# Kernel tuning notes

Hardware: AMD Instinct MI355X
Metric: run time of the kernel (lower is better)

Reference implementation:

```python
import jax, jax.numpy as jnp
import numpy as np

B, C, H, W = 8, 64, 64, 64
CK = C // 8  # query/key channels

def setup_inputs() -> dict:
    key = jax.random.key(0)
    ks = jax.random.split(key, 8)
    x = jax.random.normal(ks[0], (B, C, H, W), dtype=jnp.float32)
    # Conv1d with kernel size 1 == per-position linear map; store weights as [out, in].
    # (Spectral norm only rescales the weight matrix; with given weights the forward
    #  math is an ordinary 1x1 conv.)
    Wq = jax.random.normal(ks[1], (CK, C), dtype=jnp.float32) / np.sqrt(C)
    bq = jnp.zeros((CK,), dtype=jnp.float32)
    Wk = jax.random.normal(ks[2], (CK, C), dtype=jnp.float32) / np.sqrt(C)
    bk = jnp.zeros((CK,), dtype=jnp.float32)
    Wv = jax.random.normal(ks[3], (C, C), dtype=jnp.float32) / np.sqrt(C)
    bv = jnp.zeros((C,), dtype=jnp.float32)
    gamma = jnp.asarray(0.5, dtype=jnp.float32)  # nonzero so attention path matters
    return {"x": x, "Wq": Wq, "bq": bq, "Wk": Wk, "bk": bk, "Wv": Wv, "bv": bv, "gamma": gamma}

def reference(x, Wq, bq, Wk, bk, Wv, bv, gamma):
    b, c, h, w = x.shape
    flat = x.reshape(b, c, h * w)                       # [B, C, L]
    q = jnp.einsum('oc,bcl->blo', Wq, flat) + bq        # [B, L, C/8] (query permuted)
    k = jnp.einsum('oc,bcl->bol', Wk, flat) + bk[None, :, None]   # [B, C/8, L]
    v = jnp.einsum('oc,bcl->bol', Wv, flat) + bv[None, :, None]   # [B, C, L]
    qk = jnp.einsum('blo,bom->blm', q, k)               # [B, L, L]
    attn = jax.nn.softmax(qk, axis=1)                   # softmax over dim 1 (rows)
    out = jnp.einsum('bcl,blm->bcm', v, attn)           # [B, C, L]
    out = out.reshape(b, c, h, w)
    return gamma * out + x
```

## Files before the change

kernel.cpp:

```cpp
#include <hip/hip_runtime.h>
#include <math.h>

#define B_   8
#define C_   64
#define CK_  8
#define L_   4096

typedef __attribute__((ext_vector_type(8))) __bf16 bf16x8;
typedef __attribute__((ext_vector_type(4))) __bf16 bf16x4;
typedef __attribute__((ext_vector_type(4))) float  f32x4;

__global__ __launch_bounds__(256) void qkv_kernel(
    const float* __restrict__ x,
    const float* __restrict__ Wq, const float* __restrict__ bq,
    const float* __restrict__ Wk, const float* __restrict__ bk,
    const float* __restrict__ Wv, const float* __restrict__ bv,
    __bf16* __restrict__ qo, __bf16* __restrict__ ko, __bf16* __restrict__ vpack)
{
    __shared__ float LWq[CK_ * C_];
    __shared__ float LWk[CK_ * C_];
    __shared__ float LWv[C_ * C_];
    __shared__ __bf16 Lqs[64 * 8];
    __shared__ __bf16 Lks[64 * 8];

    const int tid = threadIdx.x;
    if (tid < 128) {
        ((float4*)LWq)[tid] = ((const float4*)Wq)[tid];
        ((float4*)LWk)[tid] = ((const float4*)Wk)[tid];
    }
    #pragma unroll
    for (int j = 0; j < 4; ++j)
        ((float4*)LWv)[tid + j * 256] = ((const float4*)Wv)[tid + j * 256];
    __syncthreads();

    const int b  = blockIdx.x >> 6;
    const int t  = blockIdx.x & 63;
    const int l0 = t << 6;
    const int lg = tid & 15;
    const int g  = tid >> 4;

    float va[4][4];
    float qk[4];
    #pragma unroll
    for (int j = 0; j < 4; ++j) {
        float bb = bv[4 * g + j];
        va[j][0] = bb; va[j][1] = bb; va[j][2] = bb; va[j][3] = bb;
    }
    {
        float bb = (g < 8) ? bq[g] : bk[g - 8];
        qk[0] = bb; qk[1] = bb; qk[2] = bb; qk[3] = bb;
    }
    const float* wqk = (g < 8) ? (LWq + g * C_) : (LWk + (g - 8) * C_);

    const float* xp = x + ((size_t)b * C_) * L_ + l0 + lg * 4;
    #pragma unroll 4
    for (int c4 = 0; c4 < 16; ++c4) {
        float4 xv[4];
        #pragma unroll
        for (int u = 0; u < 4; ++u)
            xv[u] = *(const float4*)(xp + (size_t)(4 * c4 + u) * L_);
        #pragma unroll
        for (int j = 0; j < 4; ++j) {
            float4 wv = ((const float4*)(LWv + (4 * g + j) * C_))[c4];
            float* a = va[j];
            a[0]=fmaf(wv.x,xv[0].x,a[0]); a[1]=fmaf(wv.x,xv[0].y,a[1]); a[2]=fmaf(wv.x,xv[0].z,a[2]); a[3]=fmaf(wv.x,xv[0].w,a[3]);
            a[0]=fmaf(wv.y,xv[1].x,a[0]); a[1]=fmaf(wv.y,xv[1].y,a[1]); a[2]=fmaf(wv.y,xv[1].z,a[2]); a[3]=fmaf(wv.y,xv[1].w,a[3]);
            a[0]=fmaf(wv.z,xv[2].x,a[0]); a[1]=fmaf(wv.z,xv[2].y,a[1]); a[2]=fmaf(wv.z,xv[2].z,a[2]); a[3]=fmaf(wv.z,xv[2].w,a[3]);
            a[0]=fmaf(wv.w,xv[3].x,a[0]); a[1]=fmaf(wv.w,xv[3].y,a[1]); a[2]=fmaf(wv.w,xv[3].z,a[2]); a[3]=fmaf(wv.w,xv[3].w,a[3]);
        }
        {
            float4 wv = ((const float4*)wqk)[c4];
            qk[0]=fmaf(wv.x,xv[0].x,qk[0]); qk[1]=fmaf(wv.x,xv[0].y,qk[1]); qk[2]=fmaf(wv.x,xv[0].z,qk[2]); qk[3]=fmaf(wv.x,xv[0].w,qk[3]);
            qk[0]=fmaf(wv.y,xv[1].x,qk[0]); qk[1]=fmaf(wv.y,xv[1].y,qk[1]); qk[2]=fmaf(wv.y,xv[1].z,qk[2]); qk[3]=fmaf(wv.y,xv[1].w,qk[3]);
            qk[0]=fmaf(wv.z,xv[2].x,qk[0]); qk[1]=fmaf(wv.z,xv[2].y,qk[1]); qk[2]=fmaf(wv.z,xv[2].z,qk[2]); qk[3]=fmaf(wv.z,xv[2].w,qk[3]);
            qk[0]=fmaf(wv.w,xv[3].x,qk[0]); qk[1]=fmaf(wv.w,xv[3].y,qk[1]); qk[2]=fmaf(wv.w,xv[3].z,qk[2]); qk[3]=fmaf(wv.w,xv[3].w,qk[3]);
        }
    }

    {
        __bf16* vt = vpack + ((size_t)b * 64 + t) * 4096;
        const int cb = g >> 2;
        const int sg = lg >> 2;
        const int qd = lg & 3;
        #pragma unroll
        for (int j = 0; j < 4; ++j) {
            bf16x4 vv;
            vv[0]=(__bf16)va[j][0]; vv[1]=(__bf16)va[j][1]; vv[2]=(__bf16)va[j][2]; vv[3]=(__bf16)va[j][3];
            *(bf16x4*)(vt + ((size_t)((cb * 4 + sg) * 64 + qd * 16 + (g & 3) * 4 + j)) * 4) = vv;
        }
    }
    #pragma unroll
    for (int u = 0; u < 4; ++u) {
        if (g < 8) Lqs[(lg * 4 + u) * 8 + g]       = (__bf16)qk[u];
        else       Lks[(lg * 4 + u) * 8 + (g - 8)] = (__bf16)qk[u];
    }
    __syncthreads();
    if (tid < 64) {
        *(bf16x8*)(qo + ((size_t)b * L_ + l0 + tid) * 8) = *(bf16x8*)(Lqs + tid * 8);
        *(bf16x8*)(ko + ((size_t)b * L_ + l0 + tid) * 8) = *(bf16x8*)(Lks + tid * 8);
    }
}

__global__ __launch_bounds__(512, 4) void attn_kernel(
    const __bf16* __restrict__ q, const __bf16* __restrict__ kT,
    const __bf16* __restrict__ VP, const float* __restrict__ x,
    const float* __restrict__ gamma_p, float* __restrict__ out)
{
    __shared__ __bf16 Lv[2][4][4096];
    __shared__ float  csA[8][16];

    const int tid  = threadIdx.x;
    const int w    = tid >> 6;
    const int lane = tid & 63;
    const int quad = lane >> 4;
    const int l16  = lane & 15;
    const int wh   = w & 3;
    const int lh   = w >> 2;
    const int mb   = blockIdx.x & 63;
    const int b    = blockIdx.x >> 6;
    const int m0   = mb << 6;

    const __bf16* vp = VP + (size_t)b * (64 * 4096);
    const __bf16* qb = q  + (size_t)b * L_ * CK_;

    bf16x8 kf = {};
    if (quad == 0) kf = *(const bf16x8*)(kT + ((size_t)b * L_ + m0 + wh * 16 + l16) * CK_);

    const __bf16* gk[4];
    int ok[4];
    #pragma unroll
    for (int k = 0; k < 4; ++k) {
        const int u = w * 4 + k, tl = u >> 3, seg = u & 7;
        gk[k] = vp + (size_t)((tl & 1) * 32 + (tl >> 1)) * 4096 + seg * 512 + lane * 8;
        ok[k] = tl * 4096 + seg * 512 + lane * 8;
    }

    f32x4 acc[4] = {};
    float csum = 0.f;
    bf16x8 r[4];

    #pragma unroll
    for (int k = 0; k < 4; ++k) r[k] = *(const bf16x8*)gk[k];
    #pragma unroll
    for (int k = 0; k < 4; ++k) *(bf16x8*)(&Lv[0][0][0] + ok[k]) = r[k];

    for (int i = 0; i < 16; ++i) {
        __syncthreads();

        if (i < 15) {
            #pragma unroll
            for (int k = 0; k < 4; ++k)
                r[k] = *(const bf16x8*)(gk[k] + (size_t)(i + 1) * 8192);
        }

        bf16x8 qA[4], qB[4];
        #pragma unroll
        for (int sg = 0; sg < 4; ++sg) {
            qA[sg] = *(const bf16x8*)(qb + (size_t)((lh * 32 + 2 * i)     * 64 + sg * 16 + l16) * CK_);
            qB[sg] = *(const bf16x8*)(qb + (size_t)((lh * 32 + 2 * i + 1) * 64 + sg * 16 + l16) * CK_);
        }

        bf16x4 pkA[4], pkB[4];
        #pragma unroll
        for (int sg = 0; sg < 4; ++sg) {
            f32x4 sv = __builtin_amdgcn_mfma_f32_16x16x32_bf16(qA[sg], kf, (f32x4){0.f,0.f,0.f,0.f}, 0, 0, 0);
            const float e0 = __expf(sv[0]);
            const float e1 = __expf(sv[1]);
            const float e2 = __expf(sv[2]);
            const float e3 = __expf(sv[3]);
            csum += (e0 + e1) + (e2 + e3);
            pkA[sg][0]=(__bf16)e0; pkA[sg][1]=(__bf16)e1; pkA[sg][2]=(__bf16)e2; pkA[sg][3]=(__bf16)e3;
        }
        #pragma unroll
        for (int sg = 0; sg < 4; ++sg) {
            f32x4 sv = __builtin_amdgcn_mfma_f32_16x16x32_bf16(qB[sg], kf, (f32x4){0.f,0.f,0.f,0.f}, 0, 0, 0);
            const float e0 = __expf(sv[0]);
            const float e1 = __expf(sv[1]);
            const float e2 = __expf(sv[2]);
            const float e3 = __expf(sv[3]);
            csum += (e0 + e1) + (e2 + e3);
            pkB[sg][0]=(__bf16)e0; pkB[sg][1]=(__bf16)e1; pkB[sg][2]=(__bf16)e2; pkB[sg][3]=(__bf16)e3;
        }

        const __bf16* LbA = &Lv[i & 1][lh][0];
        const __bf16* LbB = &Lv[i & 1][2 + lh][0];
        #pragma unroll
        for (int sg = 0; sg < 4; ++sg) {
            bf16x8 p8 = __builtin_shufflevector(pkA[sg], pkB[sg], 0, 1, 2, 3, 4, 5, 6, 7);
            #pragma unroll
            for (int cb = 0; cb < 4; ++cb) {
                bf16x4 vfA = *(const bf16x4*)(LbA + ((size_t)((cb * 4 + sg) * 64 + lane)) * 4);
                bf16x4 vfB = *(const bf16x4*)(LbB + ((size_t)((cb * 4 + sg) * 64 + lane)) * 4);
                bf16x8 a8 = __builtin_shufflevector(vfA, vfB, 0, 1, 2, 3, 4, 5, 6, 7);
                acc[cb] = __builtin_amdgcn_mfma_f32_16x16x32_bf16(a8, p8, acc[cb], 0, 0, 0);
            }
        }

        if (i < 15) {
            const int nb = (i + 1) & 1;
            #pragma unroll
            for (int k = 0; k < 4; ++k)
                *(bf16x8*)(&Lv[nb][0][0] + ok[k]) = r[k];
        }
    }

    float* Sc = (float*)&Lv[0][0][0];
    if (lh == 1) {
        #pragma unroll
        for (int cb = 0; cb < 4; ++cb)
            #pragma unroll
            for (int r2 = 0; r2 < 4; ++r2)
                Sc[(wh * 64 + cb * 16 + quad * 4 + r2) * 16 + l16] = acc[cb][r2];
    }
    csum += __shfl_xor(csum, 16);
    csum += __shfl_xor(csum, 32);
    if (quad == 0) csA[w][l16] = csum;
    __syncthreads();

    if (lh == 0) {
        const float rinv = gamma_p[0] / (csA[wh][l16] + csA[wh + 4][l16]);
        #pragma unroll
        for (int cb = 0; cb < 4; ++cb) {
            #pragma unroll
            for (int r2 = 0; r2 < 4; ++r2) {
                const int c = cb * 16 + quad * 4 + r2;
                const float vsum = acc[cb][r2] + Sc[(wh * 64 + c) * 16 + l16];
                const size_t idx = ((size_t)(b * 64 + c)) * L_ + m0 + wh * 16 + l16;
                out[idx] = fmaf(rinv, vsum, x[idx]);
            }
        }
    }
}

extern "C" void kernel_launch(void* const* d_in, const int* in_sizes, int n_in,
                              void* d_out, int out_size, void* d_ws, size_t ws_size,
                              hipStream_t stream) {
    const float* x  = (const float*)d_in[0];
    const float* Wq = (const float*)d_in[1];
    const float* bq = (const float*)d_in[2];
    const float* Wk = (const float*)d_in[3];
    const float* bk = (const float*)d_in[4];
    const float* Wv = (const float*)d_in[5];
    const float* bv = (const float*)d_in[6];
    const float* gm = (const float*)d_in[7];
    float* out = (float*)d_out;

    __bf16* ws    = (__bf16*)d_ws;
    __bf16* qo    = ws;
    __bf16* ko    = ws + 262144;
    __bf16* vpack = ws + 524288;

    qkv_kernel<<<dim3(B_ * (L_ / 64)), dim3(256), 0, stream>>>(
        x, Wq, bq, Wk, bk, Wv, bv, qo, ko, vpack);
    attn_kernel<<<dim3(B_ * 64), dim3(512), 0, stream>>>(
        qo, ko, vpack, x, gm, out);
}
```

Measured before the change: 126.8 us.

## Split attention l-range four ways with two m-tiles per wave

Reworks the attention kernel's wave decomposition. Each wave now computes two 16-column m-tiles, which lets one V fragment from LDS feed two MFMAs. The l dimension is split across four wave groups instead of two, each with its own private single-buffered LDS V slab, and partial results are reduced through shared memory at the end. This halves LDS V reads per MFMA but replaces double buffering with two barriers per iteration, adds a wider cross-group reduction, and raises register use.

```diff
diff --git a/kernel.cpp b/kernel.cpp
--- a/kernel.cpp
+++ b/kernel.cpp
@@ -106,16 +106,16 @@
     const __bf16* __restrict__ VP, const float* __restrict__ x,
     const float* __restrict__ gamma_p, float* __restrict__ out)
 {
-    __shared__ __bf16 Lv[2][4][4096];
-    __shared__ float  csA[8][16];
+    __shared__ __bf16 Lv[4][2][4096];
+    __shared__ float  csA[16][16];
 
     const int tid  = threadIdx.x;
     const int w    = tid >> 6;
     const int lane = tid & 63;
     const int quad = lane >> 4;
     const int l16  = lane & 15;
-    const int wh   = w & 3;
-    const int lh   = w >> 2;
+    const int wh   = w & 1;
+    const int lh   = w >> 1;
     const int mb   = blockIdx.x & 63;
     const int b    = blockIdx.x >> 6;
     const int m0   = mb << 6;
@@ -123,110 +123,123 @@
     const __bf16* vp = VP + (size_t)b * (64 * 4096);
     const __bf16* qb = q  + (size_t)b * L_ * CK_;
 
-    bf16x8 kf = {};
-    if (quad == 0) kf = *(const bf16x8*)(kT + ((size_t)b * L_ + m0 + wh * 16 + l16) * CK_);
-
-    const __bf16* gk[4];
-    int ok[4];
-    #pragma unroll
-    for (int k = 0; k < 4; ++k) {
-        const int u = w * 4 + k, tl = u >> 3, seg = u & 7;
-        gk[k] = vp + (size_t)((tl & 1) * 32 + (tl >> 1)) * 4096 + seg * 512 + lane * 8;
-        ok[k] = tl * 4096 + seg * 512 + lane * 8;
-    }
-
-    f32x4 acc[4] = {};
-    float csum = 0.f;
-    bf16x8 r[4];
-
-    #pragma unroll
-    for (int k = 0; k < 4; ++k) r[k] = *(const bf16x8*)gk[k];
-    #pragma unroll
-    for (int k = 0; k < 4; ++k) *(bf16x8*)(&Lv[0][0][0] + ok[k]) = r[k];
-
-    for (int i = 0; i < 16; ++i) {
-        __syncthreads();
-
-        if (i < 15) {
-            #pragma unroll
-            for (int k = 0; k < 4; ++k)
-                r[k] = *(const bf16x8*)(gk[k] + (size_t)(i + 1) * 8192);
-        }
-
+    bf16x8 kf0 = {}, kf1 = {};
+    if (quad == 0) {
+        kf0 = *(const bf16x8*)(kT + ((size_t)b * L_ + m0 + wh * 32 + l16) * CK_);
+        kf1 = *(const bf16x8*)(kT + ((size_t)b * L_ + m0 + wh * 32 + 16 + l16) * CK_);
+    }
+
+    const __bf16* gs = vp + ((size_t)(lh * 16 + wh)) * 4096 + lane * 8;
+    __bf16* Ld = &Lv[lh][wh][0] + lane * 8;
+
+    f32x4 acc0[4] = {}, acc1[4] = {};
+    float csum0 = 0.f, csum1 = 0.f;
+    bf16x8 r[8];
+
+    #pragma unroll
+    for (int k = 0; k < 8; ++k) r[k] = *(const bf16x8*)(gs + k * 512);
+    #pragma unroll
+    for (int k = 0; k < 8; ++k) *(bf16x8*)(Ld + k * 512) = r[k];
+    __syncthreads();
+
+    for (int i = 0; i < 8; ++i) {
+        if (i < 7) {
+            #pragma unroll
+            for (int k = 0; k < 8; ++k)
+                r[k] = *(const bf16x8*)(gs + (size_t)(2 * (i + 1)) * 4096 + k * 512);
+        }
+
+        const int te = lh * 16 + 2 * i;
         bf16x8 qA[4], qB[4];
         #pragma unroll
         for (int sg = 0; sg < 4; ++sg) {
-            qA[sg] = *(const bf16x8*)(qb + (size_t)((lh * 32 + 2 * i)     * 64 + sg * 16 + l16) * CK_);
-            qB[sg] = *(const bf16x8*)(qb + (size_t)((lh * 32 + 2 * i + 1) * 64 + sg * 16 + l16) * CK_);
-        }
-
-        bf16x4 pkA[4], pkB[4];
+            qA[sg] = *(const bf16x8*)(qb + (size_t)(te * 64 + sg * 16 + l16) * CK_);
+            qB[sg] = *(const bf16x8*)(qb + (size_t)((te + 1) * 64 + sg * 16 + l16) * CK_);
+        }
+
+        const __bf16* LbA = &Lv[lh][0][0];
+        const __bf16* LbB = &Lv[lh][1][0];
         #pragma unroll
         for (int sg = 0; sg < 4; ++sg) {
-            f32x4 sv = __builtin_amdgcn_mfma_f32_16x16x32_bf16(qA[sg], kf, (f32x4){0.f,0.f,0.f,0.f}, 0, 0, 0);
-            const float e0 = __expf(sv[0]);
-            const float e1 = __expf(sv[1]);
-            const float e2 = __expf(sv[2]);
-            const float e3 = __expf(sv[3]);
-            csum += (e0 + e1) + (e2 + e3);
-            pkA[sg][0]=(__bf16)e0; pkA[sg][1]=(__bf16)e1; pkA[sg][2]=(__bf16)e2; pkA[sg][3]=(__bf16)e3;
-        }
-        #pragma unroll
-        for (int sg = 0; sg < 4; ++sg) {
-            f32x4 sv = __builtin_amdgcn_mfma_f32_16x16x32_bf16(qB[sg], kf, (f32x4){0.f,0.f,0.f,0.f}, 0, 0, 0);
-            const float e0 = __expf(sv[0]);
-            const float e1 = __expf(sv[1]);
-            const float e2 = __expf(sv[2]);
-            const float e3 = __expf(sv[3]);
-            csum += (e0 + e1) + (e2 + e3);
-            pkB[sg][0]=(__bf16)e0; pkB[sg][1]=(__bf16)e1; pkB[sg][2]=(__bf16)e2; pkB[sg][3]=(__bf16)e3;
-        }
-
-        const __bf16* LbA = &Lv[i & 1][lh][0];
-        const __bf16* LbB = &Lv[i & 1][2 + lh][0];
-        #pragma unroll
-        for (int sg = 0; sg < 4; ++sg) {
-            bf16x8 p8 = __builtin_shufflevector(pkA[sg], pkB[sg], 0, 1, 2, 3, 4, 5, 6, 7);
+            f32x4 svA0 = __builtin_amdgcn_mfma_f32_16x16x32_bf16(qA[sg], kf0, (f32x4){0.f,0.f,0.f,0.f}, 0, 0, 0);
+            f32x4 svB0 = __builtin_amdgcn_mfma_f32_16x16x32_bf16(qB[sg], kf0, (f32x4){0.f,0.f,0.f,0.f}, 0, 0, 0);
+            f32x4 svA1 = __builtin_amdgcn_mfma_f32_16x16x32_bf16(qA[sg], kf1, (f32x4){0.f,0.f,0.f,0.f}, 0, 0, 0);
+            f32x4 svB1 = __builtin_amdgcn_mfma_f32_16x16x32_bf16(qB[sg], kf1, (f32x4){0.f,0.f,0.f,0.f}, 0, 0, 0);
+
+            bf16x4 pA0, pB0, pA1, pB1;
+            #pragma unroll
+            for (int r2 = 0; r2 < 4; ++r2) {
+                const float eA0 = __expf(svA0[r2]);
+                const float eB0 = __expf(svB0[r2]);
+                const float eA1 = __expf(svA1[r2]);
+                const float eB1 = __expf(svB1[r2]);
+                csum0 += eA0 + eB0;
+                csum1 += eA1 + eB1;
+                pA0[r2] = (__bf16)eA0; pB0[r2] = (__bf16)eB0;
+                pA1[r2] = (__bf16)eA1; pB1[r2] = (__bf16)eB1;
+            }
+            bf16x8 p80 = __builtin_shufflevector(pA0, pB0, 0, 1, 2, 3, 4, 5, 6, 7);
+            bf16x8 p81 = __builtin_shufflevector(pA1, pB1, 0, 1, 2, 3, 4, 5, 6, 7);
+
             #pragma unroll
             for (int cb = 0; cb < 4; ++cb) {
                 bf16x4 vfA = *(const bf16x4*)(LbA + ((size_t)((cb * 4 + sg) * 64 + lane)) * 4);
                 bf16x4 vfB = *(const bf16x4*)(LbB + ((size_t)((cb * 4 + sg) * 64 + lane)) * 4);
                 bf16x8 a8 = __builtin_shufflevector(vfA, vfB, 0, 1, 2, 3, 4, 5, 6, 7);
-                acc[cb] = __builtin_amdgcn_mfma_f32_16x16x32_bf16(a8, p8, acc[cb], 0, 0, 0);
-            }
-        }
-
-        if (i < 15) {
-            const int nb = (i + 1) & 1;
-            #pragma unroll
-            for (int k = 0; k < 4; ++k)
-                *(bf16x8*)(&Lv[nb][0][0] + ok[k]) = r[k];
-        }
-    }
-
+                acc0[cb] = __builtin_amdgcn_mfma_f32_16x16x32_bf16(a8, p80, acc0[cb], 0, 0, 0);
+                acc1[cb] = __builtin_amdgcn_mfma_f32_16x16x32_bf16(a8, p81, acc1[cb], 0, 0, 0);
+            }
+        }
+
+        if (i < 7) {
+            __syncthreads();
+            #pragma unroll
+            for (int k = 0; k < 8; ++k) *(bf16x8*)(Ld + k * 512) = r[k];
+            __syncthreads();
+        }
+    }
+
+    __syncthreads();
     float* Sc = (float*)&Lv[0][0][0];
-    if (lh == 1) {
-        #pragma unroll
-        for (int cb = 0; cb < 4; ++cb)
-            #pragma unroll
-            for (int r2 = 0; r2 < 4; ++r2)
-                Sc[(wh * 64 + cb * 16 + quad * 4 + r2) * 16 + l16] = acc[cb][r2];
-    }
-    csum += __shfl_xor(csum, 16);
-    csum += __shfl_xor(csum, 32);
-    if (quad == 0) csA[w][l16] = csum;
-    __syncthreads();
-
-    if (lh == 0) {
-        const float rinv = gamma_p[0] / (csA[wh][l16] + csA[wh + 4][l16]);
+    if (lh >= 1) {
+        float* S = Sc + (size_t)(lh - 1) * 4096;
         #pragma unroll
         for (int cb = 0; cb < 4; ++cb) {
             #pragma unroll
             for (int r2 = 0; r2 < 4; ++r2) {
                 const int c = cb * 16 + quad * 4 + r2;
-                const float vsum = acc[cb][r2] + Sc[(wh * 64 + c) * 16 + l16];
-                const size_t idx = ((size_t)(b * 64 + c)) * L_ + m0 + wh * 16 + l16;
-                out[idx] = fmaf(rinv, vsum, x[idx]);
+                S[c * 64 + wh * 32 + l16]      = acc0[cb][r2];
+                S[c * 64 + wh * 32 + 16 + l16] = acc1[cb][r2];
+            }
+        }
+    }
+    csum0 += __shfl_xor(csum0, 16);
+    csum0 += __shfl_xor(csum0, 32);
+    csum1 += __shfl_xor(csum1, 16);
+    csum1 += __shfl_xor(csum1, 32);
+    if (quad == 0) {
+        csA[lh * 4 + wh * 2 + 0][l16] = csum0;
+        csA[lh * 4 + wh * 2 + 1][l16] = csum1;
+    }
+    __syncthreads();
+
+    if (lh == 0) {
+        const float g0 = gamma_p[0];
+        const float rinv0 = g0 / (csA[wh * 2 + 0][l16] + csA[4 + wh * 2 + 0][l16]
+                                + csA[8 + wh * 2 + 0][l16] + csA[12 + wh * 2 + 0][l16]);
+        const float rinv1 = g0 / (csA[wh * 2 + 1][l16] + csA[4 + wh * 2 + 1][l16]
+                                + csA[8 + wh * 2 + 1][l16] + csA[12 + wh * 2 + 1][l16]);
+        #pragma unroll
+        for (int cb = 0; cb < 4; ++cb) {
+            #pragma unroll
+            for (int r2 = 0; r2 < 4; ++r2) {
+                const int c = cb * 16 + quad * 4 + r2;
+                const int moff0 = c * 64 + wh * 32 + l16;
+                float v0 = acc0[cb][r2] + Sc[moff0] + Sc[4096 + moff0] + Sc[8192 + moff0];
+                float v1 = acc1[cb][r2] + Sc[moff0 + 16] + Sc[4096 + moff0 + 16] + Sc[8192 + moff0 + 16];
+                const size_t idx0 = ((size_t)(b * 64 + c)) * L_ + m0 + wh * 32 + l16;
+                out[idx0]      = fmaf(rinv0, v0, x[idx0]);
+                out[idx0 + 16] = fmaf(rinv1, v1, x[idx0 + 16]);
             }
         }
     }
```

Measured after the change: 190.4 us. +50.2%, slower.
